# Kernel optimization log

Measured on AMD Instinct MI355X. Metric: run time of the kernel, lower is better.

## Reference

```python
import jax, jax.numpy as jnp
import numpy as np

N, E = 50000, 800000
IN_DIM, HIDDEN, HEADS, EDGE_DIM, OUT_DIM = 128, 64, 4, 16, 1
NEG_SLOPE = 0.2


def gat_conv(x, src, dst, edge_attr, W, We, att_src, att_dst, att_edge, bias, heads, out_ch, concat):
    n = x.shape[0]
    h = (x @ W).reshape(n, heads, out_ch)                     # [N,H,C]
    a_src = jnp.einsum('nhc,hc->nh', h, att_src)              # [N,H]
    a_dst = jnp.einsum('nhc,hc->nh', h, att_dst)
    e = (edge_attr @ We).reshape(-1, heads, out_ch)           # [E,H,C]
    a_e = jnp.einsum('ehc,hc->eh', e, att_edge)               # [E,H]
    alpha = jax.nn.leaky_relu(a_src[src] + a_dst[dst] + a_e, NEG_SLOPE)  # [E,H]
    # per-destination-node softmax
    amax = jax.ops.segment_max(alpha, dst, num_segments=n)
    ex = jnp.exp(alpha - amax[dst])
    denom = jax.ops.segment_sum(ex, dst, num_segments=n)
    alpha = ex / (denom[dst] + 1e-16)
    msg = h[src] * alpha[..., None]                           # [E,H,C]
    out = jax.ops.segment_sum(msg, dst, num_segments=n)       # [N,H,C]
    out = out.reshape(n, heads * out_ch) if concat else out.mean(axis=1)
    return out + bias


def setup_inputs() -> dict:
    key = jax.random.key(0)
    ks = jax.random.split(key, 16)
    s = 0.1
    inp = {
        'x': jax.random.normal(ks[0], (N, IN_DIM), jnp.float32),
        'edge_index': jax.random.randint(ks[1], (2, E), 0, N, jnp.int32),
        'edge_attr': jax.random.normal(ks[2], (E, EDGE_DIM), jnp.float32),
        # layer 1: heads=4, concat=True
        'W1': jax.random.normal(ks[3], (IN_DIM, HEADS * HIDDEN), jnp.float32) * s,
        'We1': jax.random.normal(ks[4], (EDGE_DIM, HEADS * HIDDEN), jnp.float32) * s,
        'as1': jax.random.normal(ks[5], (HEADS, HIDDEN), jnp.float32) * s,
        'ad1': jax.random.normal(ks[6], (HEADS, HIDDEN), jnp.float32) * s,
        'ae1': jax.random.normal(ks[7], (HEADS, HIDDEN), jnp.float32) * s,
        'b1': jnp.zeros((HEADS * HIDDEN,), jnp.float32),
        # layer 2: heads=1, concat=False
        'W2': jax.random.normal(ks[8], (HEADS * HIDDEN, HIDDEN), jnp.float32) * s,
        'We2': jax.random.normal(ks[9], (EDGE_DIM, HIDDEN), jnp.float32) * s,
        'as2': jax.random.normal(ks[10], (1, HIDDEN), jnp.float32) * s,
        'ad2': jax.random.normal(ks[11], (1, HIDDEN), jnp.float32) * s,
        'ae2': jax.random.normal(ks[12], (1, HIDDEN), jnp.float32) * s,
        'b2': jnp.zeros((HIDDEN,), jnp.float32),
        'Wlin': jax.random.normal(ks[13], (HIDDEN, OUT_DIM), jnp.float32) * s,
        'blin': jnp.zeros((OUT_DIM,), jnp.float32),
    }
    return inp


def reference(x, edge_index, edge_attr, W1, We1, as1, ad1, ae1, b1, W2, We2, as2, ad2, ae2, b2, Wlin, blin):
    src, dst = edge_index[0], edge_index[1]
    h = jax.nn.relu(gat_conv(x, src, dst, edge_attr, W1, We1, as1, ad1, ae1, b1, HEADS, HIDDEN, True))
    h = jax.nn.relu(gat_conv(h, src, dst, edge_attr, W2, We2, as2, ad2, ae2, b2, 1, HIDDEN, False))
    return h @ Wlin + blin
```

## Files before the change

### kernel.cpp

```cpp
#include <hip/hip_runtime.h>
#include <math.h>

#define IN_DIM 128
#define HID 64
#define HEADS 4
#define EDGE_DIM 16
#define L1_OUT 256
#define NEG_SLOPE 0.2f
#define PAD 64

typedef __attribute__((ext_vector_type(8))) _Float16 half8_t;
typedef __attribute__((ext_vector_type(4))) _Float16 half4_t;
typedef __attribute__((ext_vector_type(4))) float floatx4;

__global__ __launch_bounds__(256) void prep_kernel(
    const float* __restrict__ W1, const float* __restrict__ as1, const float* __restrict__ ad1,
    const float* __restrict__ W2, const float* __restrict__ as2, const float* __restrict__ ad2,
    const float* __restrict__ We1, const float* __restrict__ ae1,
    const float* __restrict__ We2, const float* __restrict__ ae2,
    _Float16* __restrict__ W1t, _Float16* __restrict__ W2t,
    float* __restrict__ q1, float* __restrict__ q2) {
    int id = blockIdx.x * 256 + threadIdx.x;
    if (id < 272 * 128) {
        int n = id >> 7, k = id & 127;
        float v = 0.f;
        if (n < 256) v = W1[k * 256 + n];
        else if (n < 260) { int h = n - 256; float s = 0.f;
            for (int c = 0; c < 64; ++c) s += W1[k * 256 + h * 64 + c] * as1[h * 64 + c]; v = s; }
        else if (n < 264) { int h = n - 260; float s = 0.f;
            for (int c = 0; c < 64; ++c) s += W1[k * 256 + h * 64 + c] * ad1[h * 64 + c]; v = s; }
        W1t[id] = (_Float16)v;
        return;
    }
    id -= 272 * 128;
    if (id < 80 * 256) {
        int n = id >> 8, k = id & 255;
        float v = 0.f;
        if (n < 64) v = W2[k * 64 + n];
        else if (n == 64) { float s = 0.f; for (int c = 0; c < 64; ++c) s += W2[k * 64 + c] * as2[c]; v = s; }
        else if (n == 65) { float s = 0.f; for (int c = 0; c < 64; ++c) s += W2[k * 64 + c] * ad2[c]; v = s; }
        W2t[id] = (_Float16)v;
        return;
    }
    id -= 80 * 256;
    if (id < 64) {
        int k = id >> 2, h = id & 3;
        float s = 0.f;
        for (int c = 0; c < 64; ++c) s += We1[k * 256 + h * 64 + c] * ae1[h * 64 + c];
        q1[id] = s;
        return;
    }
    id -= 64;
    if (id < 16) {
        float s = 0.f;
        for (int c = 0; c < 64; ++c) s += We2[id * 64 + c] * ae2[c];
        q2[id] = s;
    }
}

__global__ __launch_bounds__(256) void scatter_edge_kernel(
    const int* __restrict__ src, const int* __restrict__ dst,
    const float* __restrict__ ea, const float* __restrict__ q1,
    const float* __restrict__ q2, int* __restrict__ deg,
    float4* __restrict__ rec, int E) {
    __shared__ float q[80];
    if (threadIdx.x < 64) q[threadIdx.x] = q1[threadIdx.x];
    else if (threadIdx.x < 80) q[threadIdx.x] = q2[threadIdx.x - 64];
    __syncthreads();
    int e = blockIdx.x * 256 + threadIdx.x;
    if (e >= E) return;
    const float4* p = (const float4*)(ea + (size_t)e * EDGE_DIM);
    float4 v0 = p[0], v1 = p[1], v2 = p[2], v3 = p[3];
    int sn = src[e];
    int d = dst[e];
    float a[16] = {v0.x, v0.y, v0.z, v0.w, v1.x, v1.y, v1.z, v1.w,
                   v2.x, v2.y, v2.z, v2.w, v3.x, v3.y, v3.z, v3.w};
    float4 r1;
    float* rp = (float*)&r1;
#pragma unroll
    for (int h = 0; h < 4; ++h) {
        float s = 0.f;
#pragma unroll
        for (int k = 0; k < 16; ++k) s += a[k] * q[k * 4 + h];
        rp[h] = s;
    }
    float r2 = 0.f;
#pragma unroll
    for (int k = 0; k < 16; ++k) r2 += a[k] * q[64 + k];
    int rank = atomicAdd(&deg[d], 1);
    if (rank >= PAD) return;
    size_t pos = (size_t)d * PAD + rank;
    float4 lo;
    lo.x = __int_as_float(sn); lo.y = r2; lo.z = 0.f; lo.w = 0.f;
    rec[pos * 2] = lo;
    rec[pos * 2 + 1] = r1;
}

template <int NTOT, int NFEAT, int HATT, bool A32>
__global__ __launch_bounds__(256) void gemm_att_kernel(
    const void* __restrict__ Av, const _Float16* __restrict__ Bt,
    _Float16* __restrict__ C, float* __restrict__ asrc, float* __restrict__ adst,
    int M, int K) {
    __shared__ _Float16 As[64][72];
    __shared__ _Float16 Bts[NTOT * 16][72];
    const int tid = threadIdx.x;
    const int lane = tid & 63;
    const int w = tid >> 6;
    const int row0 = blockIdx.x * 64;
    const int m = lane & 15;
    const int quad = lane >> 4;

    floatx4 acc[NTOT];
#pragma unroll
    for (int t = 0; t < NTOT; ++t) acc[t] = (floatx4){0.f, 0.f, 0.f, 0.f};

    const int ar = tid >> 2;
    const int ac = (tid & 3) * 16;

    for (int k0 = 0; k0 < K; k0 += 64) {
        half8_t a0 = {}, a1 = {};
        if (row0 + ar < M) {
            if constexpr (A32) {
                const float* A = (const float*)Av + (size_t)(row0 + ar) * K + k0 + ac;
                const float4* f = (const float4*)A;
                float4 f0 = f[0], f1 = f[1], f2 = f[2], f3 = f[3];
                a0 = (half8_t){(_Float16)f0.x, (_Float16)f0.y, (_Float16)f0.z, (_Float16)f0.w,
                               (_Float16)f1.x, (_Float16)f1.y, (_Float16)f1.z, (_Float16)f1.w};
                a1 = (half8_t){(_Float16)f2.x, (_Float16)f2.y, (_Float16)f2.z, (_Float16)f2.w,
                               (_Float16)f3.x, (_Float16)f3.y, (_Float16)f3.z, (_Float16)f3.w};
            } else {
                const half8_t* g = (const half8_t*)((const _Float16*)Av + (size_t)(row0 + ar) * K + k0 + ac);
                a0 = g[0]; a1 = g[1];
            }
        }
        *(half8_t*)&As[ar][ac] = a0;
        *(half8_t*)&As[ar][ac + 8] = a1;
        for (int idx = tid; idx < NTOT * 128; idx += 256) {
            int n = idx >> 3, j = (idx & 7) * 8;
            *(half8_t*)&Bts[n][j] = *(const half8_t*)(Bt + (size_t)n * K + k0 + j);
        }
        __syncthreads();
#pragma unroll
        for (int kc = 0; kc < 2; ++kc) {
            half8_t af = *(const half8_t*)&As[w * 16 + m][kc * 32 + quad * 8];
#pragma unroll
            for (int t = 0; t < NTOT; ++t) {
                half8_t bf = *(const half8_t*)&Bts[t * 16 + m][kc * 32 + quad * 8];
                acc[t] = __builtin_amdgcn_mfma_f32_16x16x32_f16(af, bf, acc[t], 0, 0, 0);
            }
        }
        __syncthreads();
    }
    const int TE = NFEAT / 16;
#pragma unroll
    for (int r = 0; r < 4; ++r) {
        int row = row0 + w * 16 + quad * 4 + r;
        if (row >= M) continue;
#pragma unroll
        for (int t = 0; t < TE; ++t)
            C[(size_t)row * NFEAT + t * 16 + m] = (_Float16)acc[t][r];
        float v = acc[TE][r];
        if (m < HATT) asrc[row * HATT + m] = v;
        else if (m < 2 * HATT) adst[row * HATT + (m - HATT)] = v;
    }
}

__global__ __launch_bounds__(256) void node1_kernel(
    const int* __restrict__ deg, const float4* __restrict__ rec,
    const float* __restrict__ asrc1, const float* __restrict__ adst1,
    const _Float16* __restrict__ h1, const float* __restrict__ b1,
    _Float16* __restrict__ hr1, int Nn) {
    int lane = threadIdx.x & 63, wv = threadIdx.x >> 6;
    int n = blockIdx.x * 4 + wv;
    if (n >= Nn) return;
    int dg = __builtin_amdgcn_readfirstlane(deg[n]);
    if (dg > PAD) dg = PAD;
    size_t s0 = (size_t)n * PAD, s1 = s0 + dg;
    const int hh = lane >> 4;
    float adn = adst1[n * 4 + hh];
    const int* reci = (const int*)rec;
    const float* recf = (const float*)rec;

    float ax = 0.f, ay = 0.f, az = 0.f, aw = 0.f, l = 0.f;
    size_t s = s0;
    for (; s + 3 < s1; s += 4) {
        int i0 = reci[(s) * 8];
        int i1 = reci[(s + 1) * 8];
        int i2 = reci[(s + 2) * 8];
        int i3 = reci[(s + 3) * 8];
        float q0 = recf[(s) * 8 + 4 + hh];
        float q1v = recf[(s + 1) * 8 + 4 + hh];
        float q2v = recf[(s + 2) * 8 + 4 + hh];
        float q3 = recf[(s + 3) * 8 + 4 + hh];
        half4_t v0 = *(const half4_t*)(h1 + (size_t)i0 * L1_OUT + lane * 4);
        half4_t v1 = *(const half4_t*)(h1 + (size_t)i1 * L1_OUT + lane * 4);
        half4_t v2 = *(const half4_t*)(h1 + (size_t)i2 * L1_OUT + lane * 4);
        half4_t v3 = *(const half4_t*)(h1 + (size_t)i3 * L1_OUT + lane * 4);
        float t0 = q0 + asrc1[i0 * 4 + hh] + adn;
        float t1 = q1v + asrc1[i1 * 4 + hh] + adn;
        float t2 = q2v + asrc1[i2 * 4 + hh] + adn;
        float t3 = q3 + asrc1[i3 * 4 + hh] + adn;
        float e0 = __expf(t0 > 0.f ? t0 : NEG_SLOPE * t0);
        float e1 = __expf(t1 > 0.f ? t1 : NEG_SLOPE * t1);
        float e2 = __expf(t2 > 0.f ? t2 : NEG_SLOPE * t2);
        float e3 = __expf(t3 > 0.f ? t3 : NEG_SLOPE * t3);
        l += (e0 + e1) + (e2 + e3);
        ax += e0 * (float)v0.x + e1 * (float)v1.x + e2 * (float)v2.x + e3 * (float)v3.x;
        ay += e0 * (float)v0.y + e1 * (float)v1.y + e2 * (float)v2.y + e3 * (float)v3.y;
        az += e0 * (float)v0.z + e1 * (float)v1.z + e2 * (float)v2.z + e3 * (float)v3.z;
        aw += e0 * (float)v0.w + e1 * (float)v1.w + e2 * (float)v2.w + e3 * (float)v3.w;
    }
    for (; s < s1; ++s) {
        int i0 = reci[s * 8];
        float q0 = recf[s * 8 + 4 + hh];
        float t0 = q0 + asrc1[i0 * 4 + hh] + adn;
        half4_t v0 = *(const half4_t*)(h1 + (size_t)i0 * L1_OUT + lane * 4);
        float e0 = __expf(t0 > 0.f ? t0 : NEG_SLOPE * t0);
        l += e0;
        ax += e0 * (float)v0.x; ay += e0 * (float)v0.y;
        az += e0 * (float)v0.z; aw += e0 * (float)v0.w;
    }
    float inv = 1.f / (l + 1e-16f);
    float4 bb = *(const float4*)(b1 + lane * 4);
    half4_t out;
    out.x = (_Float16)fmaxf(ax * inv + bb.x, 0.f);
    out.y = (_Float16)fmaxf(ay * inv + bb.y, 0.f);
    out.z = (_Float16)fmaxf(az * inv + bb.z, 0.f);
    out.w = (_Float16)fmaxf(aw * inv + bb.w, 0.f);
    *(half4_t*)(hr1 + (size_t)n * L1_OUT + lane * 4) = out;
}

__global__ __launch_bounds__(256) void node2_kernel(
    const int* __restrict__ deg, const float4* __restrict__ rec,
    const float* __restrict__ asrc2, const float* __restrict__ adst2,
    const _Float16* __restrict__ h2, const float* __restrict__ b2,
    const float* __restrict__ Wlin, const float* __restrict__ blin,
    float* __restrict__ out, int Nn) {
    int lane = threadIdx.x & 63, wv = threadIdx.x >> 6;
    int n = blockIdx.x * 4 + wv;
    if (n >= Nn) return;
    int dg = __builtin_amdgcn_readfirstlane(deg[n]);
    if (dg > PAD) dg = PAD;
    size_t s0 = (size_t)n * PAD, s1 = s0 + dg;
    float adn = adst2[n];
    const int* reci = (const int*)rec;
    const float* recf = (const float*)rec;

    float l = 0.f, acc = 0.f;
    size_t s = s0;
    for (; s + 3 < s1; s += 4) {
        int n0 = reci[(s) * 8],     n1 = reci[(s + 1) * 8];
        int n2 = reci[(s + 2) * 8], n3 = reci[(s + 3) * 8];
        float q0 = recf[(s) * 8 + 1],     q1v = recf[(s + 1) * 8 + 1];
        float q2v = recf[(s + 2) * 8 + 1], q3 = recf[(s + 3) * 8 + 1];
        float t0 = q0 + asrc2[n0] + adn;
        float t1 = q1v + asrc2[n1] + adn;
        float t2 = q2v + asrc2[n2] + adn;
        float t3 = q3 + asrc2[n3] + adn;
        float v0 = (float)h2[(size_t)n0 * HID + lane];
        float v1 = (float)h2[(size_t)n1 * HID + lane];
        float v2 = (float)h2[(size_t)n2 * HID + lane];
        float v3 = (float)h2[(size_t)n3 * HID + lane];
        float e0 = __expf(t0 > 0.f ? t0 : NEG_SLOPE * t0);
        float e1 = __expf(t1 > 0.f ? t1 : NEG_SLOPE * t1);
        float e2 = __expf(t2 > 0.f ? t2 : NEG_SLOPE * t2);
        float e3 = __expf(t3 > 0.f ? t3 : NEG_SLOPE * t3);
        l += (e0 + e1) + (e2 + e3);
        acc += e0 * v0 + e1 * v1 + e2 * v2 + e3 * v3;
    }
    for (; s < s1; ++s) {
        int n0 = reci[s * 8];
        float q0 = recf[s * 8 + 1];
        float t0 = q0 + asrc2[n0] + adn;
        float e0 = __expf(t0 > 0.f ? t0 : NEG_SLOPE * t0);
        float v0 = (float)h2[(size_t)n0 * HID + lane];
        l += e0;
        acc += e0 * v0;
    }
    float res = fmaxf(acc / (l + 1e-16f) + b2[lane], 0.f);
    float t = res * Wlin[lane];
    for (int o = 32; o > 0; o >>= 1) t += __shfl_down(t, o);
    if (lane == 0) out[n] = t + blin[0];
}

extern "C" void kernel_launch(void* const* d_in, const int* in_sizes, int n_in,
                              void* d_out, int out_size, void* d_ws, size_t ws_size,
                              hipStream_t stream) {
    const float* x    = (const float*)d_in[0];
    const int*   ei   = (const int*)d_in[1];
    const float* ea   = (const float*)d_in[2];
    const float* W1   = (const float*)d_in[3];
    const float* We1  = (const float*)d_in[4];
    const float* as1  = (const float*)d_in[5];
    const float* ad1  = (const float*)d_in[6];
    const float* ae1  = (const float*)d_in[7];
    const float* b1   = (const float*)d_in[8];
    const float* W2   = (const float*)d_in[9];
    const float* We2  = (const float*)d_in[10];
    const float* as2  = (const float*)d_in[11];
    const float* ad2  = (const float*)d_in[12];
    const float* ae2  = (const float*)d_in[13];
    const float* b2   = (const float*)d_in[14];
    const float* Wlin = (const float*)d_in[15];
    const float* blin = (const float*)d_in[16];

    const int N = in_sizes[0] / IN_DIM;
    const int E = in_sizes[1] / 2;
    const int* src = ei;
    const int* dst = ei + E;

    char* base = (char*)d_ws;
    size_t off = 0;
    auto alloc = [&](size_t bytes) -> char* {
        char* p = base + off;
        off = (off + bytes + 255) & ~(size_t)255;
        return p;
    };
    int*      deg     = (int*)alloc((size_t)N * 4);
    float*    q1      = (float*)alloc(64 * 4);
    float*    q2      = (float*)alloc(16 * 4);
    _Float16* W1t     = (_Float16*)alloc((size_t)272 * 128 * 2);
    _Float16* W2t     = (_Float16*)alloc((size_t)80 * 256 * 2);
    float4*   rec     = (float4*)alloc((size_t)N * PAD * 32);
    float*    asrc1   = (float*)alloc((size_t)N * 4 * 4);
    float*    adst1   = (float*)alloc((size_t)N * 4 * 4);
    _Float16* h1      = (_Float16*)alloc((size_t)N * L1_OUT * 2);
    _Float16* hr1     = (_Float16*)alloc((size_t)N * L1_OUT * 2);
    _Float16* h2      = (_Float16*)alloc((size_t)N * HID * 2);
    float*    asrc2   = (float*)alloc((size_t)N * 4);
    float*    adst2   = (float*)alloc((size_t)N * 4);
    (void)ws_size; (void)n_in; (void)out_size;

    hipMemsetAsync(deg, 0, (size_t)N * 4, stream);
    prep_kernel<<<218, 256, 0, stream>>>(W1, as1, ad1, W2, as2, ad2,
                                         We1, ae1, We2, ae2, W1t, W2t, q1, q2);
    scatter_edge_kernel<<<(E + 255) / 256, 256, 0, stream>>>(src, dst, ea, q1, q2, deg,
                                                             rec, E);

    int mbl = (N + 63) / 64;
    gemm_att_kernel<17, 256, 4, true><<<mbl, 256, 0, stream>>>(x, W1t, h1, asrc1, adst1,
                                                               N, IN_DIM);
    node1_kernel<<<(N + 3) / 4, 256, 0, stream>>>(deg, rec, asrc1, adst1, h1, b1, hr1, N);
    gemm_att_kernel<5, 64, 1, false><<<mbl, 256, 0, stream>>>(hr1, W2t, h2, asrc2, adst2,
                                                              N, L1_OUT);
    node2_kernel<<<(N + 3) / 4, 256, 0, stream>>>(deg, rec, asrc2, adst2, h2, b2,
                                                  Wlin, blin, (float*)d_out, N);
}
```

Baseline: 326.7 us.

## Precompute layer-1 edge attention exponentials in scatter kernel and fold degree memset

The edge scatter kernel now runs after the first GEMM. It reads asrc1/adst1 per edge and stores the finished leaky-ReLU exponential for all four heads in the edge record. node1 then uses these weights directly, dropping its per-edge asrc1 gather and the exp that 16 lanes per head each repeated. The degree-counter memset is folded into prep_kernel to save one launch. The cost is a serialization: the scatter can no longer overlap or precede the GEMM, and it adds two gathered float4 loads per edge.

```diff
diff --git a/kernel.cpp b/kernel.cpp
--- a/kernel.cpp
+++ b/kernel.cpp
@@ -19,8 +19,10 @@
     const float* __restrict__ We1, const float* __restrict__ ae1,
     const float* __restrict__ We2, const float* __restrict__ ae2,
     _Float16* __restrict__ W1t, _Float16* __restrict__ W2t,
-    float* __restrict__ q1, float* __restrict__ q2) {
+    float* __restrict__ q1, float* __restrict__ q2,
+    int* __restrict__ deg, int Nn) {
     int id = blockIdx.x * 256 + threadIdx.x;
+    if (id < Nn) deg[id] = 0;
     if (id < 272 * 128) {
         int n = id >> 7, k = id & 127;
         float v = 0.f;
@@ -61,7 +63,8 @@
 __global__ __launch_bounds__(256) void scatter_edge_kernel(
     const int* __restrict__ src, const int* __restrict__ dst,
     const float* __restrict__ ea, const float* __restrict__ q1,
-    const float* __restrict__ q2, int* __restrict__ deg,
+    const float* __restrict__ q2, const float* __restrict__ asrc1,
+    const float* __restrict__ adst1, int* __restrict__ deg,
     float4* __restrict__ rec, int E) {
     __shared__ float q[80];
     if (threadIdx.x < 64) q[threadIdx.x] = q1[threadIdx.x];
@@ -73,27 +76,37 @@
     float4 v0 = p[0], v1 = p[1], v2 = p[2], v3 = p[3];
     int sn = src[e];
     int d = dst[e];
+    float4 as4 = *(const float4*)(asrc1 + (size_t)sn * 4);
+    float4 ad4 = *(const float4*)(adst1 + (size_t)d * 4);
     float a[16] = {v0.x, v0.y, v0.z, v0.w, v1.x, v1.y, v1.z, v1.w,
                    v2.x, v2.y, v2.z, v2.w, v3.x, v3.y, v3.z, v3.w};
-    float4 r1;
-    float* rp = (float*)&r1;
+    float aeq[4];
 #pragma unroll
     for (int h = 0; h < 4; ++h) {
         float s = 0.f;
 #pragma unroll
         for (int k = 0; k < 16; ++k) s += a[k] * q[k * 4 + h];
-        rp[h] = s;
+        aeq[h] = s;
     }
     float r2 = 0.f;
 #pragma unroll
     for (int k = 0; k < 16; ++k) r2 += a[k] * q[64 + k];
+    const float* asp = (const float*)&as4;
+    const float* adp = (const float*)&ad4;
+    float4 hi;
+    float* hp = (float*)&hi;
+#pragma unroll
+    for (int h = 0; h < 4; ++h) {
+        float t = aeq[h] + asp[h] + adp[h];
+        hp[h] = __expf(t > 0.f ? t : NEG_SLOPE * t);
+    }
     int rank = atomicAdd(&deg[d], 1);
     if (rank >= PAD) return;
     size_t pos = (size_t)d * PAD + rank;
     float4 lo;
     lo.x = __int_as_float(sn); lo.y = r2; lo.z = 0.f; lo.w = 0.f;
     rec[pos * 2] = lo;
-    rec[pos * 2 + 1] = r1;
+    rec[pos * 2 + 1] = hi;
 }
 
 template <int NTOT, int NFEAT, int HATT, bool A32>
@@ -167,7 +180,6 @@
 
 __global__ __launch_bounds__(256) void node1_kernel(
     const int* __restrict__ deg, const float4* __restrict__ rec,
-    const float* __restrict__ asrc1, const float* __restrict__ adst1,
     const _Float16* __restrict__ h1, const float* __restrict__ b1,
     _Float16* __restrict__ hr1, int Nn) {
     int lane = threadIdx.x & 63, wv = threadIdx.x >> 6;
@@ -177,7 +189,6 @@
     if (dg > PAD) dg = PAD;
     size_t s0 = (size_t)n * PAD, s1 = s0 + dg;
     const int hh = lane >> 4;
-    float adn = adst1[n * 4 + hh];
     const int* reci = (const int*)rec;
     const float* recf = (const float*)rec;
 
@@ -188,22 +199,14 @@
         int i1 = reci[(s + 1) * 8];
         int i2 = reci[(s + 2) * 8];
         int i3 = reci[(s + 3) * 8];
-        float q0 = recf[(s) * 8 + 4 + hh];
-        float q1v = recf[(s + 1) * 8 + 4 + hh];
-        float q2v = recf[(s + 2) * 8 + 4 + hh];
-        float q3 = recf[(s + 3) * 8 + 4 + hh];
+        float e0 = recf[(s) * 8 + 4 + hh];
+        float e1 = recf[(s + 1) * 8 + 4 + hh];
+        float e2 = recf[(s + 2) * 8 + 4 + hh];
+        float e3 = recf[(s + 3) * 8 + 4 + hh];
         half4_t v0 = *(const half4_t*)(h1 + (size_t)i0 * L1_OUT + lane * 4);
         half4_t v1 = *(const half4_t*)(h1 + (size_t)i1 * L1_OUT + lane * 4);
         half4_t v2 = *(const half4_t*)(h1 + (size_t)i2 * L1_OUT + lane * 4);
         half4_t v3 = *(const half4_t*)(h1 + (size_t)i3 * L1_OUT + lane * 4);
-        float t0 = q0 + asrc1[i0 * 4 + hh] + adn;
-        float t1 = q1v + asrc1[i1 * 4 + hh] + adn;
-        float t2 = q2v + asrc1[i2 * 4 + hh] + adn;
-        float t3 = q3 + asrc1[i3 * 4 + hh] + adn;
-        float e0 = __expf(t0 > 0.f ? t0 : NEG_SLOPE * t0);
-        float e1 = __expf(t1 > 0.f ? t1 : NEG_SLOPE * t1);
-        float e2 = __expf(t2 > 0.f ? t2 : NEG_SLOPE * t2);
-        float e3 = __expf(t3 > 0.f ? t3 : NEG_SLOPE * t3);
         l += (e0 + e1) + (e2 + e3);
         ax += e0 * (float)v0.x + e1 * (float)v1.x + e2 * (float)v2.x + e3 * (float)v3.x;
         ay += e0 * (float)v0.y + e1 * (float)v1.y + e2 * (float)v2.y + e3 * (float)v3.y;
@@ -212,10 +215,8 @@
     }
     for (; s < s1; ++s) {
         int i0 = reci[s * 8];
-        float q0 = recf[s * 8 + 4 + hh];
-        float t0 = q0 + asrc1[i0 * 4 + hh] + adn;
+        float e0 = recf[s * 8 + 4 + hh];
         half4_t v0 = *(const half4_t*)(h1 + (size_t)i0 * L1_OUT + lane * 4);
-        float e0 = __expf(t0 > 0.f ? t0 : NEG_SLOPE * t0);
         l += e0;
         ax += e0 * (float)v0.x; ay += e0 * (float)v0.y;
         az += e0 * (float)v0.z; aw += e0 * (float)v0.w;
@@ -331,16 +332,15 @@
     float*    adst2   = (float*)alloc((size_t)N * 4);
     (void)ws_size; (void)n_in; (void)out_size;
 
-    hipMemsetAsync(deg, 0, (size_t)N * 4, stream);
     prep_kernel<<<218, 256, 0, stream>>>(W1, as1, ad1, W2, as2, ad2,
-                                         We1, ae1, We2, ae2, W1t, W2t, q1, q2);
-    scatter_edge_kernel<<<(E + 255) / 256, 256, 0, stream>>>(src, dst, ea, q1, q2, deg,
-                                                             rec, E);
+                                         We1, ae1, We2, ae2, W1t, W2t, q1, q2, deg, N);
 
     int mbl = (N + 63) / 64;
     gemm_att_kernel<17, 256, 4, true><<<mbl, 256, 0, stream>>>(x, W1t, h1, asrc1, adst1,
                                                                N, IN_DIM);
-    node1_kernel<<<(N + 3) / 4, 256, 0, stream>>>(deg, rec, asrc1, adst1, h1, b1, hr1, N);
+    scatter_edge_kernel<<<(E + 255) / 256, 256, 0, stream>>>(src, dst, ea, q1, q2,
+                                                             asrc1, adst1, deg, rec, E);
+    node1_kernel<<<(N + 3) / 4, 256, 0, stream>>>(deg, rec, h1, b1, hr1, N);
     gemm_att_kernel<5, 64, 1, false><<<mbl, 256, 0, stream>>>(hr1, W2t, h2, asrc2, adst2,
                                                               N, L1_OUT);
     node2_kernel<<<(N + 3) / 4, 256, 0, stream>>>(deg, rec, asrc2, adst2, h2, b2,
```

Measured after the change: 330.2 us. Within noise of the previous version (+1.1%).
